# Kernel optimization log

Measured on AMD Instinct MI355X. Metric: run time of the kernel, lower is better.

Reference implementation:

```python
import jax, jax.numpy as jnp
import numpy as np

DIM = 1024
NUM_HEADS = 16
HEAD_DIM = DIM // NUM_HEADS
SCALE = HEAD_DIM ** -0.5


def setup_inputs() -> dict:
    key = jax.random.key(0)
    k1, k2, k3 = jax.random.split(key, 3)
    x = jax.random.normal(k1, (2, 2048, DIM), dtype=jnp.float32)
    # nn.Linear weights: stored as [out, in]; y = x @ W.T
    w_qkv = jax.random.normal(k2, (3 * DIM, DIM), dtype=jnp.float32) * (DIM ** -0.5)
    w_proj = jax.random.normal(k3, (DIM, DIM), dtype=jnp.float32) * (DIM ** -0.5)
    return {"x": x, "w_qkv": w_qkv, "w_proj": w_proj}


def reference(x, w_qkv, w_proj):
    B, L, D = x.shape
    qkv = jnp.einsum("bld,ed->ble", x, w_qkv)  # [B, L, 3*D]
    qkv = qkv.reshape(B, L, 3, NUM_HEADS, HEAD_DIM).transpose(2, 0, 3, 1, 4)
    q, k, v = qkv[0], qkv[1], qkv[2]  # each [B, H, L, hd]
    attn = jnp.einsum("bhqd,bhkd->bhqk", q, k) * SCALE
    attn = jax.nn.softmax(attn, axis=-1)
    out = jnp.einsum("bhqk,bhkd->bhqd", attn, v)  # [B, H, L, hd]
    out = out.transpose(0, 2, 1, 3).reshape(B, L, D)
    return jnp.einsum("bld,ed->ble", out, w_proj)
```

## Files before the change

kernel.cpp:

```cpp
#include <hip/hip_runtime.h>
#include <math.h>
#include <stdint.h>

#define B_ 2
#define L_ 2048
#define D_ 1024
#define H_ 16
#define HD_ 64
#define QSCALE_ 0.1803368801f

typedef __attribute__((ext_vector_type(8))) short short8;
typedef __attribute__((ext_vector_type(4))) short short4v;
typedef __attribute__((ext_vector_type(4))) float float4v;

#if defined(__has_builtin)
#if __has_builtin(__builtin_amdgcn_exp2f)
#define EXP2F(x) __builtin_amdgcn_exp2f(x)
#endif
#endif
#ifndef EXP2F
#define EXP2F(x) exp2f(x)
#endif

__device__ __forceinline__ short f2bf(float f) {
    union { float f; unsigned u; } x; x.f = f;
    unsigned r = x.u + 0x7fffu + ((x.u >> 16) & 1u);
    return (short)(r >> 16);
}

__device__ __forceinline__ unsigned fbits(float f) {
    union { float f; unsigned u; } x; x.f = f;
    return x.u;
}

__device__ __forceinline__ unsigned pk_bf_trunc(float a, float b) {
    return __builtin_amdgcn_perm(fbits(b), fbits(a), 0x07060302u);
}

__device__ __forceinline__ void gl_lds16(const void* g, void* l) {
    __builtin_amdgcn_global_load_lds(
        (const __attribute__((address_space(1))) unsigned int*)g,
        (__attribute__((address_space(3))) unsigned int*)l, 16, 0, 0);
}

__global__ __launch_bounds__(256) void cvt_w(const float* __restrict__ wqkv,
                                             const float* __restrict__ wproj,
                                             short* __restrict__ wqkvb,
                                             short* __restrict__ wprojb) {
    int i = blockIdx.x * 256 + threadIdx.x;
    const float* in;
    short* out;
    int idx;
    if (i < 786432) { in = wqkv;  out = wqkvb;  idx = i; }
    else            { in = wproj; out = wprojb; idx = i - 786432; }
    float4 v = ((const float4*)in)[idx];
    short4v o;
    o.x = f2bf(v.x); o.y = f2bf(v.y); o.z = f2bf(v.z); o.w = f2bf(v.w);
    ((short4v*)out)[idx] = o;
}

__global__ __launch_bounds__(256) void gemm_qkv_bf16(const float* __restrict__ X,
                                                     const short* __restrict__ Bm,
                                                     short* __restrict__ Qb,
                                                     short* __restrict__ Kb,
                                                     short* __restrict__ Vb) {
    __shared__ short smem[8192];
    short* As = smem;
    short* Bs = smem + 4096;
    const int tid = threadIdx.x;
    const int w = tid >> 6, l = tid & 63;
    const int lm = l & 15, q = l >> 4;
    const int m0 = blockIdx.y * 128, n0 = blockIdx.x * 128;
    const int wm = w >> 1, wn = w & 1;

    int arow_[4], acol_[4];
#pragma unroll
    for (int j = 0; j < 4; ++j) {
        int c = tid + 256 * j;
        arow_[j] = c >> 3;
        acol_[j] = (c & 7) * 4;
    }

    float4v acc[4][4];
#pragma unroll
    for (int mt = 0; mt < 4; ++mt)
#pragma unroll
        for (int nt = 0; nt < 4; ++nt) acc[mt][nt] = (float4v){0.f, 0.f, 0.f, 0.f};

    float4 areg[4];
#pragma unroll
    for (int j = 0; j < 4; ++j)
        areg[j] = *(const float4*)(X + (size_t)(m0 + arow_[j]) * 1024 + acol_[j]);

    for (int k0 = 0; k0 < 1024; k0 += 32) {
        __syncthreads();
#pragma unroll
        for (int j = 0; j < 4; ++j) {
            short4v s4;
            s4.x = f2bf(areg[j].x); s4.y = f2bf(areg[j].y);
            s4.z = f2bf(areg[j].z); s4.w = f2bf(areg[j].w);
            *(short4v*)(As + arow_[j] * 32 + acol_[j]) = s4;
        }
#pragma unroll
        for (int t = 0; t < 2; ++t) {
            int idx8 = w * 128 + t * 64 + l;
            int row = idx8 >> 2, c8 = idx8 & 3;
            gl_lds16(Bm + (size_t)(n0 + row) * 1024 + k0 + c8 * 8, (char*)Bs + w * 2048 + t * 1024);
        }
        __syncthreads();
        if (k0 < 992) {
#pragma unroll
            for (int j = 0; j < 4; ++j)
                areg[j] = *(const float4*)(X + (size_t)(m0 + arow_[j]) * 1024 + k0 + 32 + acol_[j]);
        }
        short8 af[4], bfr[4];
#pragma unroll
        for (int mt = 0; mt < 4; ++mt)
            af[mt] = *(const short8*)(As + (wm * 64 + mt * 16 + lm) * 32 + q * 8);
#pragma unroll
        for (int nt = 0; nt < 4; ++nt)
            bfr[nt] = *(const short8*)(Bs + (wn * 64 + nt * 16 + lm) * 32 + q * 8);
#pragma unroll
        for (int mt = 0; mt < 4; ++mt)
#pragma unroll
            for (int nt = 0; nt < 4; ++nt)
                acc[mt][nt] = __builtin_amdgcn_mfma_f32_16x16x32_bf16(af[mt], bfr[nt], acc[mt][nt], 0, 0, 0);
    }

    const int which = n0 >> 10;
    if (which < 2) {
        short* dst = (which == 0) ? Qb : Kb;
        const float sc = (which == 0) ? QSCALE_ : 1.0f;
#pragma unroll
        for (int half = 0; half < 2; ++half) {
            __syncthreads();
            if (wm == half) {
#pragma unroll
                for (int mt = 0; mt < 4; ++mt)
#pragma unroll
                    for (int nt = 0; nt < 4; ++nt)
#pragma unroll
                        for (int r = 0; r < 4; ++r)
                            smem[(mt * 16 + q * 4 + r) * 128 + wn * 64 + nt * 16 + lm] =
                                f2bf(acc[mt][nt][r] * sc);
            }
            __syncthreads();
#pragma unroll
            for (int j = 0; j < 4; ++j) {
                const int x = tid + 256 * j;
                const int row = x >> 4, c = x & 15;
                short8 v = *(const short8*)(smem + row * 128 + c * 8);
                const int m = m0 + half * 64 + row;
                const int b = m >> 11, ll = m & 2047;
                const int n = n0 + c * 8;
                const int hh = (n & 1023) >> 6, d = n & 63;
                *(short8*)(dst + (((size_t)b * H_ + hh) * L_ + ll) * HD_ + d) = v;
            }
        }
    } else {
#pragma unroll
        for (int mt = 0; mt < 4; ++mt) {
            const int m = m0 + wm * 64 + mt * 16 + q * 4;
            const int b = m >> 11, ll = m & 2047;
#pragma unroll
            for (int nt = 0; nt < 4; ++nt) {
                const int n = n0 + wn * 64 + nt * 16 + lm;
                const int h = (n & 1023) >> 6, d = n & 63;
                short4v pk;
                pk.x = f2bf(acc[mt][nt][0]); pk.y = f2bf(acc[mt][nt][1]);
                pk.z = f2bf(acc[mt][nt][2]); pk.w = f2bf(acc[mt][nt][3]);
                *(short4v*)(Vb + (((size_t)b * H_ + h) * HD_ + d) * L_ + ll) = pk;
            }
        }
    }
}

__global__ __launch_bounds__(256) void attn_mfma(const short* __restrict__ Qb,
                                                 const short* __restrict__ Kb,
                                                 const short* __restrict__ Vtg,
                                                 short* __restrict__ Ob) {
    __shared__ short KV[4 * 4096];
    __shared__ short Pt[128 * 72];

    const int tid = threadIdx.x;
    const int w = tid >> 6, l = tid & 63;
    const int lm = l & 15, q = l >> 4;
    const int qt = blockIdx.x, bh = blockIdx.y;

    const short* Qg = Qb  + ((size_t)bh * L_ + qt * 128) * HD_;
    const short* Kg = Kb  + (size_t)bh * L_ * HD_;
    const short* Vg = Vtg + (size_t)bh * HD_ * L_;

#pragma unroll
    for (int t = 0; t < 4; ++t) {
        int idx = tid + 256 * t;
        int row = idx >> 3, c = idx & 7;
        short8 v = *(const short8*)(Qg + row * 64 + c * 8);
        *(short8*)(Pt + row * 64 + ((c ^ (row & 7)) * 8)) = v;
    }

    const int srow = tid >> 3;
    const int sc   = tid & 7;
    const int koff0 = srow * 64 + ((sc ^ (srow & 7)) * 8);
    const int koff1 = koff0 + 32 * 64;

    {
        short8 ka = *(const short8*)(Kg + (size_t)srow * 64 + sc * 8);
        short8 kb = *(const short8*)(Kg + (size_t)(srow + 32) * 64 + sc * 8);
        short8 va = *(const short8*)(Vg + (size_t)srow * L_ + sc * 8);
        short8 vb = *(const short8*)(Vg + (size_t)(srow + 32) * L_ + sc * 8);
        *(short8*)(KV + koff0) = ka;
        *(short8*)(KV + koff1) = kb;
        *(short8*)(KV + 4096 + koff0) = va;
        *(short8*)(KV + 4096 + koff1) = vb;
    }
    short8 kra = *(const short8*)(Kg + (size_t)(64 + srow) * 64 + sc * 8);
    short8 krb = *(const short8*)(Kg + (size_t)(64 + srow + 32) * 64 + sc * 8);
    short8 vra = *(const short8*)(Vg + (size_t)srow * L_ + 64 + sc * 8);
    short8 vrb = *(const short8*)(Vg + (size_t)(srow + 32) * L_ + 64 + sc * 8);

    __syncthreads();

    short8 qf[2][2];
#pragma unroll
    for (int nq = 0; nq < 2; ++nq)
#pragma unroll
        for (int kh = 0; kh < 2; ++kh) {
            int row = w * 32 + nq * 16 + lm;
            int ch = kh * 4 + q;
            qf[nq][kh] = *(const short8*)(Pt + row * 64 + ((ch ^ (row & 7)) * 8));
        }

    int offA0[4], offA1[4], offV[2][4];
#pragma unroll
    for (int nt = 0; nt < 4; ++nt) {
        const int arow = nt * 16 + lm;
        offA0[nt] = arow * 64 + ((q ^ (arow & 7)) * 8);
        offA1[nt] = arow * 64 + (((4 + q) ^ (arow & 7)) * 8);
#pragma unroll
        for (int kh = 0; kh < 2; ++kh)
            offV[kh][nt] = arow * 64 + (((kh * 4 + q) ^ (arow & 7)) * 8);
    }

    float4v o[4][2];
#pragma unroll
    for (int mt = 0; mt < 4; ++mt)
#pragma unroll
        for (int nq = 0; nq < 2; ++nq) o[mt][nq] = (float4v){0.f, 0.f, 0.f, 0.f};
    float lsum[2] = {0.f, 0.f};

    const int prow = w * 32 + lm;

#pragma unroll 2
    for (int t = 0; t < 32; ++t) {
        const int cur = t & 1;
        short* Kl = KV + cur * 8192;
        short* Vt = Kl + 4096;
        short* Kn = KV + (1 - cur) * 8192;
        short* Vn = Kn + 4096;

        __syncthreads();

        if (t < 31) {
            *(short8*)(Kn + koff0) = kra;
            *(short8*)(Kn + koff1) = krb;
            *(short8*)(Vn + koff0) = vra;
            *(short8*)(Vn + koff1) = vrb;
        }
        if (t < 30) {
            kra = *(const short8*)(Kg + (size_t)((t + 2) * 64 + srow) * 64 + sc * 8);
            krb = *(const short8*)(Kg + (size_t)((t + 2) * 64 + srow + 32) * 64 + sc * 8);
            vra = *(const short8*)(Vg + (size_t)srow * L_ + (t + 2) * 64 + sc * 8);
            vrb = *(const short8*)(Vg + (size_t)(srow + 32) * L_ + (t + 2) * 64 + sc * 8);
        }

        float4v st[4][2];
#pragma unroll
        for (int nt = 0; nt < 4; ++nt) {
            short8 a0 = *(const short8*)(Kl + offA0[nt]);
            short8 a1 = *(const short8*)(Kl + offA1[nt]);
#pragma unroll
            for (int nq = 0; nq < 2; ++nq) {
                float4v z = (float4v){0.f, 0.f, 0.f, 0.f};
                z = __builtin_amdgcn_mfma_f32_16x16x32_bf16(a0, qf[nq][0], z, 0, 0, 0);
                z = __builtin_amdgcn_mfma_f32_16x16x32_bf16(a1, qf[nq][1], z, 0, 0, 0);
                st[nt][nq] = z;
            }
        }

#pragma unroll
        for (int nt = 0; nt < 4; ++nt)
#pragma unroll
            for (int nq = 0; nq < 2; ++nq) {
                const float e0 = EXP2F(st[nt][nq][0]);
                const float e1 = EXP2F(st[nt][nq][1]);
                const float e2 = EXP2F(st[nt][nq][2]);
                const float e3 = EXP2F(st[nt][nq][3]);
                lsum[nq] += (e0 + e1) + (e2 + e3);
                uint2 pk;
                pk.x = pk_bf_trunc(e0, e1);
                pk.y = pk_bf_trunc(e2, e3);
                *(uint2*)(Pt + (prow + nq * 16) * 72 + nt * 16 + q * 4) = pk;
            }

#pragma unroll
        for (int kh = 0; kh < 2; ++kh) {
            short8 pb[2];
#pragma unroll
            for (int nq = 0; nq < 2; ++nq)
                pb[nq] = *(const short8*)(Pt + (prow + nq * 16) * 72 + kh * 32 + q * 8);
#pragma unroll
            for (int mt = 0; mt < 4; ++mt) {
                short8 va = *(const short8*)(Vt + offV[kh][mt]);
#pragma unroll
                for (int nq = 0; nq < 2; ++nq)
                    o[mt][nq] = __builtin_amdgcn_mfma_f32_16x16x32_bf16(va, pb[nq], o[mt][nq], 0, 0, 0);
            }
        }
    }

    float inv[2];
#pragma unroll
    for (int nq = 0; nq < 2; ++nq) {
        float s = lsum[nq];
        s += __shfl_xor(s, 16);
        s += __shfl_xor(s, 32);
        inv[nq] = 1.f / s;
    }
    short* OgBase = Ob + ((size_t)bh * L_ + qt * 128) * HD_;
#pragma unroll
    for (int nq = 0; nq < 2; ++nq) {
        const int qrow = w * 32 + nq * 16 + lm;
#pragma unroll
        for (int mt = 0; mt < 4; ++mt) {
            short4v pk;
            pk.x = f2bf(o[mt][nq][0] * inv[nq]);
            pk.y = f2bf(o[mt][nq][1] * inv[nq]);
            pk.z = f2bf(o[mt][nq][2] * inv[nq]);
            pk.w = f2bf(o[mt][nq][3] * inv[nq]);
            *(short4v*)(OgBase + (size_t)qrow * 64 + mt * 16 + q * 4) = pk;
        }
    }
}

__global__ __launch_bounds__(256) void gemm_proj_bf16(const short* __restrict__ Ob,
                                                      const short* __restrict__ Wp,
                                                      float* __restrict__ out) {
    __shared__ short As[64 * 32];
    __shared__ short Bs[128 * 32];
    const int tid = threadIdx.x;
    const int w = tid >> 6, l = tid & 63;
    const int lm = l & 15, q = l >> 4;
    const int m0 = blockIdx.y * 64, n0 = blockIdx.x * 128;
    const int wm = w & 1, wn = w >> 1;
    const int b = m0 >> 11, l0 = m0 & 2047;

    float4v acc[2][4];
#pragma unroll
    for (int mt = 0; mt < 2; ++mt)
#pragma unroll
        for (int nt = 0; nt < 4; ++nt) acc[mt][nt] = (float4v){0.f, 0.f, 0.f, 0.f};

    for (int k0 = 0; k0 < 1024; k0 += 32) {
        __syncthreads();
        {
            int idx8 = w * 64 + l;
            int row = idx8 >> 2, c8 = idx8 & 3;
            int h = k0 >> 6, d = (k0 & 32) + c8 * 8;
            gl_lds16(Ob + (((size_t)b * H_ + h) * L_ + l0 + row) * HD_ + d, (char*)As + w * 1024);
        }
#pragma unroll
        for (int t = 0; t < 2; ++t) {
            int idx8 = w * 128 + t * 64 + l;
            int row = idx8 >> 2, c8 = idx8 & 3;
            gl_lds16(Wp + (size_t)(n0 + row) * 1024 + k0 + c8 * 8, (char*)Bs + w * 2048 + t * 1024);
        }
        __syncthreads();
        short8 af[2], bfr[4];
#pragma unroll
        for (int mt = 0; mt < 2; ++mt)
            af[mt] = *(const short8*)(As + (wm * 32 + mt * 16 + lm) * 32 + q * 8);
#pragma unroll
        for (int nt = 0; nt < 4; ++nt)
            bfr[nt] = *(const short8*)(Bs + (wn * 64 + nt * 16 + lm) * 32 + q * 8);
#pragma unroll
        for (int mt = 0; mt < 2; ++mt)
#pragma unroll
            for (int nt = 0; nt < 4; ++nt)
                acc[mt][nt] = __builtin_amdgcn_mfma_f32_16x16x32_bf16(af[mt], bfr[nt], acc[mt][nt], 0, 0, 0);
    }

#pragma unroll
    for (int mt = 0; mt < 2; ++mt)
#pragma unroll
        for (int nt = 0; nt < 4; ++nt)
#pragma unroll
            for (int r = 0; r < 4; ++r) {
                const int m = m0 + wm * 32 + mt * 16 + q * 4 + r;
                const int n = n0 + wn * 64 + nt * 16 + lm;
                out[(size_t)m * 1024 + n] = acc[mt][nt][r];
            }
}

extern "C" void kernel_launch(void* const* d_in, const int* in_sizes, int n_in,
                              void* d_out, int out_size, void* d_ws, size_t ws_size,
                              hipStream_t stream) {
    (void)in_sizes; (void)n_in; (void)out_size; (void)ws_size;
    const float* x      = (const float*)d_in[0];
    const float* w_qkv  = (const float*)d_in[1];
    const float* w_proj = (const float*)d_in[2];

    char* ws = (char*)d_ws;
    short* Ob     = (short*)(ws);
    short* wqkvb  = (short*)(ws + (8u  << 20));
    short* wprojb = (short*)(ws + (14u << 20));
    short* Qb     = (short*)(ws + (16u << 20));
    short* Kb     = (short*)(ws + (24u << 20));
    short* Vb     = (short*)(ws + (32u << 20));

    cvt_w<<<4096, 256, 0, stream>>>(w_qkv, w_proj, wqkvb, wprojb);
    gemm_qkv_bf16 <<<dim3(24, 32), 256, 0, stream>>>(x, wqkvb, Qb, Kb, Vb);
    attn_mfma     <<<dim3(16, 32), 256, 0, stream>>>(Qb, Kb, Vb, Ob);
    gemm_proj_bf16<<<dim3(8, 64),  256, 0, stream>>>(Ob, wprojb, (float*)d_out);
}
```

Measured before the change: 208.5 us.

## Pre-convert X to bf16 and remap GEMM blocks for XCD locality

Converts the input activations to bf16 in the same elementwise kernel that converts the weights. The QKV GEMM can then load its A tile with direct global-to-LDS copies instead of loading fp32 into registers and converting in the loop. Both GEMMs switch to a 1D grid with block indices remapped so that blocks on the same XCD share N tiles, which should improve L2 reuse. The cost is an extra 8 MB write and 8 MB read of bf16 X, and the removal of the register prefetch of A, which used to overlap its load with compute.

New measurement: 198.1 us. -5.0%, faster.

```diff
diff --git a/kernel.cpp b/kernel.cpp
--- a/kernel.cpp
+++ b/kernel.cpp
@@ -43,23 +43,26 @@
         (__attribute__((address_space(3))) unsigned int*)l, 16, 0, 0);
 }
 
-__global__ __launch_bounds__(256) void cvt_w(const float* __restrict__ wqkv,
-                                             const float* __restrict__ wproj,
-                                             short* __restrict__ wqkvb,
-                                             short* __restrict__ wprojb) {
+__global__ __launch_bounds__(256) void cvt_all(const float* __restrict__ x,
+                                               const float* __restrict__ wqkv,
+                                               const float* __restrict__ wproj,
+                                               short* __restrict__ xb,
+                                               short* __restrict__ wqkvb,
+                                               short* __restrict__ wprojb) {
     int i = blockIdx.x * 256 + threadIdx.x;
     const float* in;
     short* out;
     int idx;
-    if (i < 786432) { in = wqkv;  out = wqkvb;  idx = i; }
-    else            { in = wproj; out = wprojb; idx = i - 786432; }
+    if (i < 1048576)      { in = x;     out = xb;     idx = i; }
+    else if (i < 1835008) { in = wqkv;  out = wqkvb;  idx = i - 1048576; }
+    else                  { in = wproj; out = wprojb; idx = i - 1835008; }
     float4 v = ((const float4*)in)[idx];
     short4v o;
     o.x = f2bf(v.x); o.y = f2bf(v.y); o.z = f2bf(v.z); o.w = f2bf(v.w);
     ((short4v*)out)[idx] = o;
 }
 
-__global__ __launch_bounds__(256) void gemm_qkv_bf16(const float* __restrict__ X,
+__global__ __launch_bounds__(256) void gemm_qkv_bf16(const short* __restrict__ A,
                                                      const short* __restrict__ Bm,
                                                      short* __restrict__ Qb,
                                                      short* __restrict__ Kb,
@@ -70,49 +73,30 @@
     const int tid = threadIdx.x;
     const int w = tid >> 6, l = tid & 63;
     const int lm = l & 15, q = l >> 4;
-    const int m0 = blockIdx.y * 128, n0 = blockIdx.x * 128;
+    const int bid = blockIdx.x;
+    const int xcd = bid & 7;
+    const int grp = bid >> 3;
+    const int n_tile = xcd + 8 * (grp % 3);
+    const int m_tile = grp / 3;
+    const int m0 = m_tile * 128, n0 = n_tile * 128;
     const int wm = w >> 1, wn = w & 1;
 
-    int arow_[4], acol_[4];
-#pragma unroll
-    for (int j = 0; j < 4; ++j) {
-        int c = tid + 256 * j;
-        arow_[j] = c >> 3;
-        acol_[j] = (c & 7) * 4;
-    }
-
     float4v acc[4][4];
 #pragma unroll
     for (int mt = 0; mt < 4; ++mt)
 #pragma unroll
         for (int nt = 0; nt < 4; ++nt) acc[mt][nt] = (float4v){0.f, 0.f, 0.f, 0.f};
-
-    float4 areg[4];
-#pragma unroll
-    for (int j = 0; j < 4; ++j)
-        areg[j] = *(const float4*)(X + (size_t)(m0 + arow_[j]) * 1024 + acol_[j]);
 
     for (int k0 = 0; k0 < 1024; k0 += 32) {
         __syncthreads();
-#pragma unroll
-        for (int j = 0; j < 4; ++j) {
-            short4v s4;
-            s4.x = f2bf(areg[j].x); s4.y = f2bf(areg[j].y);
-            s4.z = f2bf(areg[j].z); s4.w = f2bf(areg[j].w);
-            *(short4v*)(As + arow_[j] * 32 + acol_[j]) = s4;
-        }
 #pragma unroll
         for (int t = 0; t < 2; ++t) {
             int idx8 = w * 128 + t * 64 + l;
             int row = idx8 >> 2, c8 = idx8 & 3;
+            gl_lds16(A  + (size_t)(m0 + row) * 1024 + k0 + c8 * 8, (char*)As + w * 2048 + t * 1024);
             gl_lds16(Bm + (size_t)(n0 + row) * 1024 + k0 + c8 * 8, (char*)Bs + w * 2048 + t * 1024);
         }
         __syncthreads();
-        if (k0 < 992) {
-#pragma unroll
-            for (int j = 0; j < 4; ++j)
-                areg[j] = *(const float4*)(X + (size_t)(m0 + arow_[j]) * 1024 + k0 + 32 + acol_[j]);
-        }
         short8 af[4], bfr[4];
 #pragma unroll
         for (int mt = 0; mt < 4; ++mt)
@@ -351,7 +335,8 @@
     const int tid = threadIdx.x;
     const int w = tid >> 6, l = tid & 63;
     const int lm = l & 15, q = l >> 4;
-    const int m0 = blockIdx.y * 64, n0 = blockIdx.x * 128;
+    const int bid = blockIdx.x;
+    const int m0 = (bid >> 3) * 64, n0 = (bid & 7) * 128;
     const int wm = w & 1, wn = w >> 1;
     const int b = m0 >> 11, l0 = m0 & 2047;
 
@@ -411,15 +396,16 @@
     const float* w_proj = (const float*)d_in[2];
 
     char* ws = (char*)d_ws;
-    short* Ob     = (short*)(ws);
+    short* xb     = (short*)(ws);
     short* wqkvb  = (short*)(ws + (8u  << 20));
     short* wprojb = (short*)(ws + (14u << 20));
     short* Qb     = (short*)(ws + (16u << 20));
     short* Kb     = (short*)(ws + (24u << 20));
     short* Vb     = (short*)(ws + (32u << 20));
-
-    cvt_w<<<4096, 256, 0, stream>>>(w_qkv, w_proj, wqkvb, wprojb);
-    gemm_qkv_bf16 <<<dim3(24, 32), 256, 0, stream>>>(x, wqkvb, Qb, Kb, Vb);
+    short* Ob     = (short*)(ws + (40u << 20));
+
+    cvt_all<<<8192, 256, 0, stream>>>(x, w_qkv, w_proj, xb, wqkvb, wprojb);
+    gemm_qkv_bf16 <<<768, 256, 0, stream>>>(xb, wqkvb, Qb, Kb, Vb);
     attn_mfma     <<<dim3(16, 32), 256, 0, stream>>>(Qb, Kb, Vb, Ob);
-    gemm_proj_bf16<<<dim3(8, 64),  256, 0, stream>>>(Ob, wprojb, (float*)d_out);
-}
+    gemm_proj_bf16<<<512, 256, 0, stream>>>(Ob, wprojb, (float*)d_out);
+}
```
